# Kernel optimization log

Hardware: AMD Instinct MI355X
Metric: run time of the kernel (lower is better)

Reference implementation:

```python
import jax, jax.numpy as jnp
import numpy as np

NUM_CLASSES = 8   # num_input_classes
BIN_SIZE = 640
K = 16            # num_neighbors
HID = 256         # hidden_dim
DDIM = 128        # distance_dim
MAX_BINS = 200


def setup_inputs() -> dict:
    key = jax.random.key(0)
    ks = jax.random.split(key, 16)
    B, N, F = 4, 12800, 16
    X = jax.random.normal(ks[0], (B, N, F), jnp.float32)
    ids = jax.random.randint(ks[1], (B, N), 0, NUM_CLASSES).astype(jnp.float32)
    X = X.at[:, :, 0].set(ids)
    d_in = NUM_CLASSES + (F - 1)  # 23 after one-hot encoding

    def w(k, shp):
        return jax.random.normal(k, shp, jnp.float32) * 0.05

    return {
        "X": X,
        # point-embedding FFN (layer_encoding): Dense(128, elu) -> Dense(DDIM)
        "We1": w(ks[2], (d_in, 128)), "be1": jnp.zeros((128,), jnp.float32),
        "We2": w(ks[3], (128, DDIM)), "be2": jnp.zeros((DDIM,), jnp.float32),
        # edge FFN (layer_edge): Dense(128, elu) -> Dense(1)
        "Wd1": w(ks[4], (2 * d_in + 1, 128)), "bd1": jnp.zeros((128,), jnp.float32),
        "Wd2": w(ks[5], (128, 1)), "bd2": jnp.zeros((1,), jnp.float32),
        # LSH codebook random rotations (DDIM, max_num_bins//2)
        "R": w(ks[6], (DDIM, MAX_BINS // 2)),
        # encoder dense
        "Wenc": w(ks[7], (d_in, HID)), "benc": jnp.zeros((HID,), jnp.float32),
        # GHConv weights
        "Wt": w(ks[8], (HID, HID)), "bt": jnp.zeros((HID,), jnp.float32),
        "Wh": w(ks[9], (HID, HID)),
        "theta": w(ks[10], (HID, HID)),
        # decoder dense + output head
        "Wdec": w(ks[11], (HID, HID)), "bdec": jnp.zeros((HID,), jnp.float32),
        "Wout": w(ks[12], (HID, 3)), "bout": jnp.zeros((3,), jnp.float32),
    }


def _ffn(x, W1, b1, W2, b2):
    return jax.nn.elu(x @ W1 + b1) @ W2 + b2


def _build_edges(pe, R):
    # pe: (N, DDIM) point embeddings for one event
    N = pe.shape[0]
    nbins = N // BIN_SIZE
    mul = pe @ R[:, : nbins // 2]                      # (N, nbins//2)
    cmul = jnp.concatenate([mul, -mul], axis=-1)       # (N, nbins)
    # LSH binning: argsort of argmax bin id -> (nbins, BIN_SIZE) node indices
    bins = jnp.argsort(jnp.argmax(cmul, axis=-1)).reshape(nbins, BIN_SIZE)
    parts = pe[bins]                                   # (nbins, bs, DDIM)
    dm = jax.nn.sigmoid(jnp.einsum('bif,bjf->bij', parts, parts))
    vals, idx = jax.lax.top_k(dm, K)                   # (nbins, bs, K)
    src = jnp.broadcast_to(bins[:, :, None], (nbins, BIN_SIZE, K)).reshape(-1)
    dst = bins[jnp.arange(nbins)[:, None, None], idx].reshape(-1)
    return src, dst, vals.reshape(-1)


def _ghconv(x, src, dst, w, Wt, bt, Wh, theta):
    # x: (N, HID); edge list (src, dst, w) of length E; out[src] += w * h[dst]
    N = x.shape[0]
    deg = jax.ops.segment_sum(jnp.abs(w), src, num_segments=N)
    norm = (deg + 1e-6) ** -0.5                        # (N,)
    f_hom = (x @ theta) * norm[:, None]
    agg = jax.ops.segment_sum(w[:, None] * f_hom[dst], src, num_segments=N)
    agg = agg * norm[:, None]
    gate = jax.nn.sigmoid(x @ Wt + bt)
    return jax.nn.selu(gate * agg + (1.0 - gate) * (x @ Wh))


def reference(X, We1, be1, We2, be2, Wd1, bd1, Wd2, bd2, R, Wenc, benc, Wt, bt, Wh, theta, Wdec, bdec, Wout, bout):
    # InputEncoding: one-hot the class id, keep remaining properties
    ids = jax.nn.one_hot(X[..., 0].astype(jnp.int32), NUM_CLASSES, dtype=X.dtype)
    h0 = jnp.concatenate([ids, X[..., 1:]], axis=-1)   # (B, N, 23)
    # SparseHashedNNDistance: embed points, LSH-bin, per-bin kNN, edge net
    pe = _ffn(h0, We1, be1, We2, be2)                  # (B, N, DDIM)
    src, dst, d = jax.vmap(lambda p: _build_edges(p, R))(pe)   # each (B, N*K)
    x1 = jax.vmap(lambda h, s: h[s])(h0, src)
    x2 = jax.vmap(lambda h, s: h[s])(h0, dst)
    ef = jnp.concatenate([x1, x2, d[..., None]], axis=-1)      # (B, E, 47)
    w = jax.nn.sigmoid(_ffn(ef, Wd1, bd1, Wd2, bd2))[..., 0]   # (B, E) edge weights
    # EncoderDecoderGNN: Dense encoder -> GHConv -> Dense decoder -> head
    xe = jax.nn.selu(h0 @ Wenc + benc)                 # (B, N, HID)
    xg = jax.vmap(lambda x, s, t, ww: _ghconv(x, s, t, ww, Wt, bt, Wh, theta))(xe, src, dst, w)
    xd = jax.nn.selu(xg @ Wdec + bdec)
    return xd @ Wout + bout                            # (B, N, 3)
```

## Files before the change

### kernel.cpp

```cpp
#include <hip/hip_runtime.h>
#include <cstdint>
#include <cstddef>
#include <math.h>

#define BB    4
#define NN    12800
#define FF    16
#define DIN   23
#define NCLS  8
#define DDIM  128
#define HID   256
#define NBINS 20
#define BS    640
#define KNB   16
#define EE    (NN*KNB)
#define BN    (BB*NN)

__device__ __forceinline__ float eluf(float x){ return x > 0.f ? x : expm1f(x); }
__device__ __forceinline__ float seluf(float x){
  const float a = 1.6732632423543772f, s = 1.0507009873554805f;
  return x > 0.f ? s*x : s*a*expm1f(x);
}
__device__ __forceinline__ float sigf(float x){ return 1.f/(1.f+expf(-x)); }

__global__ void k_h0(const float* __restrict__ X, float* __restrict__ h0){
  int id = blockIdx.x*256 + threadIdx.x;
  if (id >= BN*DIN) return;
  int p = id / DIN, f = id % DIN;
  const float* xr = X + (size_t)p*FF;
  float v;
  if (f < NCLS){
    int cls = (int)xr[0];
    v = (f == cls) ? 1.f : 0.f;
  } else {
    v = xr[f - NCLS + 1];
  }
  h0[id] = v;
}

__global__ void k_pe(const float* __restrict__ h0,
                     const float* __restrict__ We1, const float* __restrict__ be1,
                     const float* __restrict__ We2, const float* __restrict__ be2,
                     float* __restrict__ pe){
  __shared__ double hid[2][128];
  int t = threadIdx.x;
  int lp = t >> 7, j = t & 127;
  size_t p = (size_t)blockIdx.x*2 + lp;
  const float* hr = h0 + p*DIN;
  double acc = (double)be1[j];
  #pragma unroll
  for (int k=0;k<DIN;++k) acc += (double)hr[k]*(double)We1[k*DDIM + j];
  hid[lp][j] = acc > 0.0 ? acc : expm1(acc);
  __syncthreads();
  double acc2 = (double)be2[j];
  #pragma unroll 8
  for (int k=0;k<DDIM;++k) acc2 += hid[lp][k]*(double)We2[k*DDIM + j];
  pe[p*DDIM + j] = (float)acc2;
}

__global__ void k_binid(const float* __restrict__ pe, const float* __restrict__ R,
                        int* __restrict__ bid){
  int tid = blockIdx.x*256 + threadIdx.x;
  int p = tid >> 2, part = tid & 3;
  const float* pr = pe + (size_t)p*DDIM + part*32;
  double m[10];
  #pragma unroll
  for (int j=0;j<10;++j) m[j] = 0.0;
  #pragma unroll 4
  for (int k=0;k<32;++k){
    double v = (double)pr[k];
    const float* rr = R + (size_t)(part*32 + k)*100;
    #pragma unroll
    for (int j=0;j<10;++j) m[j] += v*(double)rr[j];
  }
  #pragma unroll
  for (int j=0;j<10;++j){
    m[j] += __shfl_xor(m[j], 1);
    m[j] += __shfl_xor(m[j], 2);
  }
  if (part == 0){
    float mf[10];
    #pragma unroll
    for (int j=0;j<10;++j) mf[j] = (float)m[j];
    float bv = -1e30f; int bi = 0;
    #pragma unroll
    for (int j=0;j<20;++j){
      float v = (j<10) ? mf[j] : -mf[j-10];
      if (v > bv){ bv = v; bi = j; }
    }
    bid[p] = bi;
  }
}

__global__ void k_place(const int* __restrict__ binid, int* __restrict__ order){
  int b = blockIdx.x / NBINS, mybin = blockIdx.x % NBINS;
  const int* bid = binid + (size_t)b*NN;
  int t = threadIdx.x;
  __shared__ int wsum[4];
  __shared__ int wtot[4];
  __shared__ int sOff;
  int c = 0;
  for (int i = t; i < NN; i += 256) c += (bid[i] < mybin) ? 1 : 0;
  #pragma unroll
  for (int o=32;o;o>>=1) c += __shfl_xor(c, o);
  if ((t & 63) == 0) wsum[t >> 6] = c;
  __syncthreads();
  if (t == 0) sOff = wsum[0]+wsum[1]+wsum[2]+wsum[3];
  __syncthreads();
  int base = sOff;
  int lane = t & 63, w = t >> 6;
  for (int ch = 0; ch < NN; ch += 256){
    int i = ch + t;
    bool flag = (i < NN) && (bid[i] == mybin);
    unsigned long long bal = __ballot(flag);
    int pre = __popcll(bal & ((1ull << lane) - 1ull));
    if (lane == 0) wtot[w] = __popcll(bal);
    __syncthreads();
    int woff = 0;
    #pragma unroll
    for (int ww=0; ww<4; ++ww) if (ww < w) woff += wtot[ww];
    if (flag) order[(size_t)b*NN + base + woff + pre] = i;
    base += wtot[0]+wtot[1]+wtot[2]+wtot[3];
    __syncthreads();
  }
}

#define TP 68
__global__ void __launch_bounds__(256)
k_topk(const float* __restrict__ pe, const int* __restrict__ order,
       float* __restrict__ valk, int* __restrict__ idxk){
  __shared__ float rowT[64][TP];
  __shared__ float colT[64][TP];
  __shared__ float S[64][69];
  __shared__ unsigned short midx[64][48];
  __shared__ int ordRow[64];
  __shared__ int ordCol[64];
  int blk = blockIdx.x;
  int b   = blk / (NBINS*10);
  int rem = blk % (NBINS*10);
  int bin = rem / 10, rt = rem % 10;
  int r0 = rt*64;
  int t = threadIdx.x;
  const float* peb = pe + (size_t)b*NN*DDIM;
  const int* ob = order + (size_t)b*NN + (size_t)bin*BS;
  if (t < 64) ordRow[t] = ob[r0 + t];

  float tv[16]; int ti[16];
  #pragma unroll
  for (int j=0;j<16;++j){ tv[j] = -1e30f; ti[j] = 1<<20; }
  float wv = -1e30f; int wi = 1<<20; int wpos = 0;

  int tm = t & 15, tn = t >> 4;
  int rsel = t & 63, qsel = t >> 6;

  for (int ct = 0; ct < 10; ++ct){
    __syncthreads();
    if (t < 64) ordCol[t] = ob[ct*64 + t];
    double acc[4][4];
    #pragma unroll
    for (int i=0;i<4;++i){
      #pragma unroll
      for (int j=0;j<4;++j) acc[i][j] = 0.0;
    }
    #pragma unroll
    for (int kh = 0; kh < 2; ++kh){
      __syncthreads();
      for (int l=t; l<4096; l+=256){
        int rr = l >> 6, kk = l & 63;
        rowT[kk][rr] = peb[(size_t)ordRow[rr]*DDIM + kh*64 + kk];
      }
      for (int l=t; l<4096; l+=256){
        int cc = l >> 6, kk = l & 63;
        colT[kk][cc] = peb[(size_t)ordCol[cc]*DDIM + kh*64 + kk];
      }
      __syncthreads();
      #pragma unroll 4
      for (int kk=0; kk<64; ++kk){
        float4 a = *(const float4*)&rowT[kk][4*tm];
        float4 w = *(const float4*)&colT[kk][4*tn];
        double ad[4], wd[4];
        ad[0]=(double)a.x; ad[1]=(double)a.y; ad[2]=(double)a.z; ad[3]=(double)a.w;
        wd[0]=(double)w.x; wd[1]=(double)w.y; wd[2]=(double)w.z; wd[3]=(double)w.w;
        #pragma unroll
        for (int i=0;i<4;++i){
          #pragma unroll
          for (int j=0;j<4;++j) acc[i][j] += ad[i]*wd[j];
        }
      }
    }
    #pragma unroll
    for (int i=0;i<4;++i){
      #pragma unroll
      for (int j=0;j<4;++j)
        S[4*tm+i][4*tn+j] = sigf((float)acc[i][j]);
    }
    __syncthreads();
    #pragma unroll
    for (int j=0;j<16;++j){
      float v = S[rsel][qsel*16 + j];
      int gc = ct*64 + qsel*16 + j;
      bool better = (v > wv) || (v == wv && gc < wi);
      if (better){
        #pragma unroll
        for (int u=0;u<16;++u){ if (u == wpos){ tv[u] = v; ti[u] = gc; } }
        wv = tv[0]; wi = ti[0]; wpos = 0;
        #pragma unroll
        for (int u=1;u<16;++u){
          bool worse = (tv[u] < wv) || (tv[u] == wv && ti[u] > wi);
          if (worse){ wv = tv[u]; wi = ti[u]; wpos = u; }
        }
      }
    }
  }
  __syncthreads();
  if (qsel > 0){
    #pragma unroll
    for (int j=0;j<16;++j){
      S[rsel][(qsel-1)*16 + j] = tv[j];
      midx[rsel][(qsel-1)*16 + j] = (unsigned short)ti[j];
    }
  }
  __syncthreads();
  if (qsel == 0){
    for (int j=0;j<48;++j){
      float v = S[rsel][j]; int gc = (int)midx[rsel][j];
      bool better = (v > wv) || (v == wv && gc < wi);
      if (better){
        #pragma unroll
        for (int u=0;u<16;++u){ if (u == wpos){ tv[u] = v; ti[u] = gc; } }
        wv = tv[0]; wi = ti[0]; wpos = 0;
        #pragma unroll
        for (int u=1;u<16;++u){
          bool worse = (tv[u] < wv) || (tv[u] == wv && ti[u] > wi);
          if (worse){ wv = tv[u]; wi = ti[u]; wpos = u; }
        }
      }
    }
    size_t base = (((size_t)(b*NBINS + bin))*BS + r0 + rsel)*KNB;
    #pragma unroll
    for (int j=0;j<16;++j){ valk[base + j] = tv[j]; idxk[base + j] = ti[j]; }
  }
}

__global__ void k_epart(const float* __restrict__ h0,
                        const float* __restrict__ Wd1, const float* __restrict__ bd1,
                        float* __restrict__ spart, float* __restrict__ dpart){
  int t = threadIdx.x;
  int lp = t >> 7, j = t & 127;
  size_t p = (size_t)blockIdx.x*2 + lp;
  const float* hr = h0 + p*DIN;
  float sa = bd1[j];
  float da = 0.f;
  #pragma unroll
  for (int k=0;k<DIN;++k){
    float x = hr[k];
    sa += x*Wd1[k*128 + j];
    da += x*Wd1[(DIN+k)*128 + j];
  }
  spart[p*128 + j] = sa;
  dpart[p*128 + j] = da;
}

__global__ void k_edges(const float* __restrict__ spart, const float* __restrict__ dpart,
                        const int* __restrict__ order,
                        const float* __restrict__ valk, const int* __restrict__ idxk,
                        const float* __restrict__ Wd1, const float* __restrict__ Wd2,
                        const float* __restrict__ bd2,
                        float* __restrict__ wgt, int* __restrict__ dste){
  int lane = threadIdx.x & 63;
  size_t e = (size_t)blockIdx.x*4 + (threadIdx.x >> 6);
  int b  = (int)(e / EE);
  int eb = (int)(e % EE);
  int bin = eb / (BS*KNB);
  int rem = eb % (BS*KNB);
  int i  = rem / KNB;
  int kk = rem % KNB;
  const int* ob = order + (size_t)b*NN + (size_t)bin*BS;
  int src = ob[i];
  size_t tkb = ((size_t)(b*NBINS + bin)*BS + i)*KNB + kk;
  int ip = idxk[tkb];
  int dst = ob[ip];
  float dv = valk[tkb];
  size_t gs = ((size_t)b*NN + src)*128;
  size_t gd = ((size_t)b*NN + dst)*128;
  float a1 = spart[gs + lane]      + dpart[gd + lane]      + dv*Wd1[46*128 + lane];
  float a2 = spart[gs + 64 + lane] + dpart[gd + 64 + lane] + dv*Wd1[46*128 + 64 + lane];
  float ptl = eluf(a1)*Wd2[lane] + eluf(a2)*Wd2[lane + 64];
  #pragma unroll
  for (int o=32;o;o>>=1) ptl += __shfl_xor(ptl, o);
  if (lane == 0){
    wgt[e]  = sigf(ptl + bd2[0]);
    dste[e] = dst;
  }
}

__global__ void k_deg(const float* __restrict__ wgt, const int* __restrict__ order,
                      float* __restrict__ nrm){
  int id = blockIdx.x*256 + threadIdx.x;
  if (id >= BN) return;
  int b = id / NN;
  int p = id % NN;
  const float* w = wgt + (size_t)b*EE + (size_t)p*KNB;
  float s = 0.f;
  #pragma unroll
  for (int k=0;k<KNB;++k) s += fabsf(w[k]);
  int node = order[id];
  nrm[(size_t)b*NN + node] = 1.f/sqrtf(s + 1e-6f);
}

__global__ void k_enc(const float* __restrict__ h0, const float* __restrict__ Wenc,
                      const float* __restrict__ benc, float* __restrict__ xe){
  __shared__ float hs[8][DIN+1];
  size_t p0 = (size_t)blockIdx.x*8;
  int t = threadIdx.x;
  if (t < 8*DIN){
    int pp = t / DIN, ff = t - pp*DIN;
    hs[pp][ff] = h0[(p0+pp)*DIN + ff];
  }
  float wreg[DIN];
  #pragma unroll
  for (int k=0;k<DIN;++k) wreg[k] = Wenc[k*HID + t];
  float bb = benc[t];
  __syncthreads();
  #pragma unroll
  for (int pp=0;pp<8;++pp){
    float acc = bb;
    #pragma unroll
    for (int k=0;k<DIN;++k) acc += hs[pp][k]*wreg[k];
    xe[(p0+pp)*HID + t] = seluf(acc);
  }
}

template<int MODE>
__global__ void __launch_bounds__(256)
k_gemm128(const float* __restrict__ A, const float* __restrict__ W,
          const float* __restrict__ bias, const float* __restrict__ rs,
          float* __restrict__ C){
  __shared__ float As[16][132];
  __shared__ float Ws[16][132];
  int t = threadIdx.x;
  int m0 = blockIdx.x*128, n0 = blockIdx.y*128;
  int tx = t & 15, ty = t >> 4;
  float acc[8][8];
  #pragma unroll
  for (int i=0;i<8;++i){
    #pragma unroll
    for (int j=0;j<8;++j) acc[i][j] = 0.f;
  }
  for (int kt=0; kt<16; ++kt){
    int k0 = kt*16;
    __syncthreads();
    #pragma unroll
    for (int l=0;l<8;++l){
      int idx = t + l*256;
      int m = idx >> 4, kk = idx & 15;
      As[kk][m] = A[((size_t)(m0+m))*HID + k0 + kk];
    }
    #pragma unroll
    for (int l=0;l<8;++l){
      int idx = t + l*256;
      int kk = idx >> 7, nn = idx & 127;
      Ws[kk][nn] = W[((size_t)(k0+kk))*HID + n0 + nn];
    }
    __syncthreads();
    #pragma unroll
    for (int kk=0;kk<16;++kk){
      float4 a0 = *(const float4*)&As[kk][4*ty];
      float4 a1 = *(const float4*)&As[kk][64 + 4*ty];
      float4 w0 = *(const float4*)&Ws[kk][4*tx];
      float4 w1 = *(const float4*)&Ws[kk][64 + 4*tx];
      float av[8], wv[8];
      av[0]=a0.x; av[1]=a0.y; av[2]=a0.z; av[3]=a0.w;
      av[4]=a1.x; av[5]=a1.y; av[6]=a1.z; av[7]=a1.w;
      wv[0]=w0.x; wv[1]=w0.y; wv[2]=w0.z; wv[3]=w0.w;
      wv[4]=w1.x; wv[5]=w1.y; wv[6]=w1.z; wv[7]=w1.w;
      #pragma unroll
      for (int i=0;i<8;++i){
        #pragma unroll
        for (int j=0;j<8;++j) acc[i][j] += av[i]*wv[j];
      }
    }
  }
  float b0[8];
  if (MODE == 2 || MODE == 3){
    #pragma unroll
    for (int j=0;j<8;++j) b0[j] = bias[n0 + (j<4 ? 4*tx+j : 60+4*tx+j)];
  }
  #pragma unroll
  for (int i=0;i<8;++i){
    int row = m0 + (i<4 ? 4*ty+i : 60+4*ty+i);
    float sc = (MODE == 1) ? rs[row] : 1.f;
    float v[8];
    #pragma unroll
    for (int j=0;j<8;++j){
      float x = acc[i][j];
      if (MODE == 2 || MODE == 3) x += b0[j];
      if (MODE == 1) x *= sc;
      if (MODE == 2) x = sigf(x);
      if (MODE == 3) x = seluf(x);
      v[j] = x;
    }
    float4 r0; r0.x=v[0]; r0.y=v[1]; r0.z=v[2]; r0.w=v[3];
    float4 r1; r1.x=v[4]; r1.y=v[5]; r1.z=v[6]; r1.w=v[7];
    *(float4*)&C[(size_t)row*HID + n0 + 4*tx]      = r0;
    *(float4*)&C[(size_t)row*HID + n0 + 64 + 4*tx] = r1;
  }
}

__global__ void k_combine(const float* __restrict__ fh, const float* __restrict__ xh,
                          const float* __restrict__ gate, const float* __restrict__ wgt,
                          const int* __restrict__ dste, const int* __restrict__ order,
                          const float* __restrict__ nrm, float* __restrict__ xg){
  __shared__ float ew[KNB];
  __shared__ int   ed[KNB];
  int blk = blockIdx.x;
  int b = blk / NN, p = blk % NN;
  int t = threadIdx.x;
  if (t < KNB){
    size_t e = (size_t)b*EE + (size_t)p*KNB + t;
    ew[t] = wgt[e];
    ed[t] = dste[e];
  }
  __syncthreads();
  int src = order[(size_t)b*NN + p];
  float nr = nrm[(size_t)b*NN + src];
  size_t base = (size_t)b*NN*HID;
  float acc = 0.f;
  #pragma unroll
  for (int k=0;k<KNB;++k) acc += ew[k]*fh[base + (size_t)ed[k]*HID + t];
  acc *= nr;
  size_t o = base + (size_t)src*HID + t;
  float g = gate[o];
  xg[o] = seluf(g*acc + (1.f - g)*xh[o]);
}

__global__ void k_head(const float* __restrict__ xd, const float* __restrict__ Wout,
                       const float* __restrict__ bout, float* __restrict__ out){
  int lane = threadIdx.x & 63;
  size_t p = (size_t)blockIdx.x*4 + (threadIdx.x >> 6);
  float4 x = *(const float4*)&xd[p*HID + lane*4];
  float a0 = 0.f, a1 = 0.f, a2 = 0.f;
  const float* wr = Wout + lane*4*3;
  a0 += x.x*wr[0]; a1 += x.x*wr[1]; a2 += x.x*wr[2];
  a0 += x.y*wr[3]; a1 += x.y*wr[4]; a2 += x.y*wr[5];
  a0 += x.z*wr[6]; a1 += x.z*wr[7]; a2 += x.z*wr[8];
  a0 += x.w*wr[9]; a1 += x.w*wr[10]; a2 += x.w*wr[11];
  #pragma unroll
  for (int o=32;o;o>>=1){
    a0 += __shfl_xor(a0, o);
    a1 += __shfl_xor(a1, o);
    a2 += __shfl_xor(a2, o);
  }
  if (lane == 0){
    out[p*3 + 0] = a0 + bout[0];
    out[p*3 + 1] = a1 + bout[1];
    out[p*3 + 2] = a2 + bout[2];
  }
}

extern "C" void kernel_launch(void* const* d_in, const int* in_sizes, int n_in,
                              void* d_out, int out_size, void* d_ws, size_t ws_size,
                              hipStream_t stream){
  (void)in_sizes; (void)n_in; (void)out_size; (void)ws_size;
  const float* X    = (const float*)d_in[0];
  const float* We1  = (const float*)d_in[1];
  const float* be1  = (const float*)d_in[2];
  const float* We2  = (const float*)d_in[3];
  const float* be2  = (const float*)d_in[4];
  const float* Wd1  = (const float*)d_in[5];
  const float* bd1  = (const float*)d_in[6];
  const float* Wd2  = (const float*)d_in[7];
  const float* bd2  = (const float*)d_in[8];
  const float* R    = (const float*)d_in[9];
  const float* Wenc = (const float*)d_in[10];
  const float* benc = (const float*)d_in[11];
  const float* Wt   = (const float*)d_in[12];
  const float* bt   = (const float*)d_in[13];
  const float* Wh   = (const float*)d_in[14];
  const float* theta= (const float*)d_in[15];
  const float* Wdec = (const float*)d_in[16];
  const float* bdec = (const float*)d_in[17];
  const float* Wout = (const float*)d_in[18];
  const float* bout = (const float*)d_in[19];
  float* out = (float*)d_out;

  char* ws = (char*)d_ws; size_t off = 0;
  auto alloc = [&](size_t bytes)->void*{
    void* p = ws + off; off = (off + bytes + 255) & ~(size_t)255; return p;
  };
  float* h0   = (float*)alloc((size_t)BN*DIN*4);
  float* pe   = (float*)alloc((size_t)BN*DDIM*4);
  int*   bid  = (int*)  alloc((size_t)BN*4);
  int*   order= (int*)  alloc((size_t)BN*4);
  float* valk = (float*)alloc((size_t)BB*NBINS*BS*KNB*4);
  int*   idxk = (int*)  alloc((size_t)BB*NBINS*BS*KNB*4);
  float* wgt  = (float*)alloc((size_t)BB*EE*4);
  int*   dste = (int*)  alloc((size_t)BB*EE*4);
  float* nrm  = (float*)alloc((size_t)BN*4);
  float* xe   = (float*)alloc((size_t)BN*HID*4);
  float* fh   = (float*)alloc((size_t)BN*HID*4);
  float* xh   = (float*)alloc((size_t)BN*HID*4);
  float* gate = (float*)alloc((size_t)BN*HID*4);
  float* spart = pe;
  float* dpart = xe;
  float* xg    = xe;
  float* xd    = fh;

  k_h0   <<<(BN*DIN + 255)/256, 256, 0, stream>>>(X, h0);
  k_pe   <<<BN/2, 256, 0, stream>>>(h0, We1, be1, We2, be2, pe);
  k_binid<<<BN*4/256, 256, 0, stream>>>(pe, R, bid);
  k_place<<<BB*NBINS, 256, 0, stream>>>(bid, order);
  k_topk <<<BB*NBINS*10, 256, 0, stream>>>(pe, order, valk, idxk);
  k_epart<<<BN/2, 256, 0, stream>>>(h0, Wd1, bd1, spart, dpart);
  k_edges<<<BB*EE/4, 256, 0, stream>>>(spart, dpart, order, valk, idxk, Wd1, Wd2, bd2, wgt, dste);
  k_deg  <<<(BN + 255)/256, 256, 0, stream>>>(wgt, order, nrm);
  k_enc  <<<BN/8, 256, 0, stream>>>(h0, Wenc, benc, xe);
  dim3 gg(BN/128, HID/128);
  k_gemm128<0><<<gg, 256, 0, stream>>>(xe, Wh,    nullptr, nullptr, xh);
  k_gemm128<1><<<gg, 256, 0, stream>>>(xe, theta, nullptr, nrm,     fh);
  k_gemm128<2><<<gg, 256, 0, stream>>>(xe, Wt,    bt,      nullptr, gate);
  k_combine<<<BN, 256, 0, stream>>>(fh, xh, gate, wgt, dste, order, nrm, xg);
  k_gemm128<3><<<gg, 256, 0, stream>>>(xg, Wdec,  bdec,    nullptr, xd);
  k_head <<<BN/4, 256, 0, stream>>>(xd, Wout, bout, out);
}
```

Measured before the change: 1.814 ms.

## Remap topk tile so each thread owns one row's 16 columns

Changes the thread-to-output mapping in the per-bin kNN kernel: each thread now computes 16 consecutive column scores for a single row instead of a 4x4 tile. The scores feed the thread's running top-16 directly from registers, which removes the shared score matrix S, its write/read pass and one barrier per column tile. The merge buffers reuse the rowT/colT shared memory, cutting the LDS footprint and possibly raising occupancy. In exchange, data reuse per LDS load drops (1 row value per 16 FMAs instead of 4x4 outer products), so more LDS traffic goes to the fp64 FMAs.

```diff
diff --git a/kernel.cpp b/kernel.cpp
--- a/kernel.cpp
+++ b/kernel.cpp
@@ -125,14 +125,12 @@
   }
 }
 
-#define TP 68
+#define TPAD 68
 __global__ void __launch_bounds__(256)
 k_topk(const float* __restrict__ pe, const int* __restrict__ order,
        float* __restrict__ valk, int* __restrict__ idxk){
-  __shared__ float rowT[64][TP];
-  __shared__ float colT[64][TP];
-  __shared__ float S[64][69];
-  __shared__ unsigned short midx[64][48];
+  __shared__ float rowT[64][TPAD];
+  __shared__ float colT[64][TPAD];
   __shared__ int ordRow[64];
   __shared__ int ordCol[64];
   int blk = blockIdx.x;
@@ -141,6 +139,8 @@
   int bin = rem / 10, rt = rem % 10;
   int r0 = rt*64;
   int t = threadIdx.x;
+  int lane = t & 63;
+  int q    = t >> 6;
   const float* peb = pe + (size_t)b*NN*DDIM;
   const int* ob = order + (size_t)b*NN + (size_t)bin*BS;
   if (t < 64) ordRow[t] = ob[r0 + t];
@@ -150,18 +150,11 @@
   for (int j=0;j<16;++j){ tv[j] = -1e30f; ti[j] = 1<<20; }
   float wv = -1e30f; int wi = 1<<20; int wpos = 0;
 
-  int tm = t & 15, tn = t >> 4;
-  int rsel = t & 63, qsel = t >> 6;
-
   for (int ct = 0; ct < 10; ++ct){
-    __syncthreads();
     if (t < 64) ordCol[t] = ob[ct*64 + t];
-    double acc[4][4];
-    #pragma unroll
-    for (int i=0;i<4;++i){
-      #pragma unroll
-      for (int j=0;j<4;++j) acc[i][j] = 0.0;
-    }
+    double acc[16];
+    #pragma unroll
+    for (int j=0;j<16;++j) acc[j] = 0.0;
     #pragma unroll
     for (int kh = 0; kh < 2; ++kh){
       __syncthreads();
@@ -174,31 +167,27 @@
         colT[kk][cc] = peb[(size_t)ordCol[cc]*DDIM + kh*64 + kk];
       }
       __syncthreads();
-      #pragma unroll 4
+      #pragma unroll 2
       for (int kk=0; kk<64; ++kk){
-        float4 a = *(const float4*)&rowT[kk][4*tm];
-        float4 w = *(const float4*)&colT[kk][4*tn];
-        double ad[4], wd[4];
-        ad[0]=(double)a.x; ad[1]=(double)a.y; ad[2]=(double)a.z; ad[3]=(double)a.w;
-        wd[0]=(double)w.x; wd[1]=(double)w.y; wd[2]=(double)w.z; wd[3]=(double)w.w;
-        #pragma unroll
-        for (int i=0;i<4;++i){
-          #pragma unroll
-          for (int j=0;j<4;++j) acc[i][j] += ad[i]*wd[j];
-        }
+        double a = (double)rowT[kk][lane];
+        float4 w0 = *(const float4*)&colT[kk][16*q];
+        float4 w1 = *(const float4*)&colT[kk][16*q + 4];
+        float4 w2 = *(const float4*)&colT[kk][16*q + 8];
+        float4 w3 = *(const float4*)&colT[kk][16*q + 12];
+        acc[0]  += a*(double)w0.x; acc[1]  += a*(double)w0.y;
+        acc[2]  += a*(double)w0.z; acc[3]  += a*(double)w0.w;
+        acc[4]  += a*(double)w1.x; acc[5]  += a*(double)w1.y;
+        acc[6]  += a*(double)w1.z; acc[7]  += a*(double)w1.w;
+        acc[8]  += a*(double)w2.x; acc[9]  += a*(double)w2.y;
+        acc[10] += a*(double)w2.z; acc[11] += a*(double)w2.w;
+        acc[12] += a*(double)w3.x; acc[13] += a*(double)w3.y;
+        acc[14] += a*(double)w3.z; acc[15] += a*(double)w3.w;
       }
     }
     #pragma unroll
-    for (int i=0;i<4;++i){
-      #pragma unroll
-      for (int j=0;j<4;++j)
-        S[4*tm+i][4*tn+j] = sigf((float)acc[i][j]);
-    }
-    __syncthreads();
-    #pragma unroll
     for (int j=0;j<16;++j){
-      float v = S[rsel][qsel*16 + j];
-      int gc = ct*64 + qsel*16 + j;
+      float v = sigf((float)acc[j]);
+      int gc = ct*64 + 16*q + j;
       bool better = (v > wv) || (v == wv && gc < wi);
       if (better){
         #pragma unroll
@@ -213,17 +202,21 @@
     }
   }
   __syncthreads();
-  if (qsel > 0){
+  float* mv = (float*)&rowT[0][0];
+  int*   mi = (int*)  &colT[0][0];
+  const int MS = 49;
+  if (q > 0){
     #pragma unroll
     for (int j=0;j<16;++j){
-      S[rsel][(qsel-1)*16 + j] = tv[j];
-      midx[rsel][(qsel-1)*16 + j] = (unsigned short)ti[j];
-    }
-  }
-  __syncthreads();
-  if (qsel == 0){
+      mv[lane*MS + (q-1)*16 + j] = tv[j];
+      mi[lane*MS + (q-1)*16 + j] = ti[j];
+    }
+  }
+  __syncthreads();
+  if (q == 0){
     for (int j=0;j<48;++j){
-      float v = S[rsel][j]; int gc = (int)midx[rsel][j];
+      float v = mv[lane*MS + j];
+      int gc  = mi[lane*MS + j];
       bool better = (v > wv) || (v == wv && gc < wi);
       if (better){
         #pragma unroll
@@ -236,7 +229,7 @@
         }
       }
     }
-    size_t base = (((size_t)(b*NBINS + bin))*BS + r0 + rsel)*KNB;
+    size_t base = (((size_t)(b*NBINS + bin))*BS + r0 + lane)*KNB;
     #pragma unroll
     for (int j=0;j<16;++j){ valk[base + j] = tv[j]; idxk[base + j] = ti[j]; }
   }
```

Measured after the change: 1.746 ms. -3.8%, faster.

## Use fp32 accumulation in topk GEMM, load row tile once, reuse shared memory

Applied to the files above, without the earlier changes.

Switches the per-bin similarity accumulation in k_topk from double to float, which is much cheaper on the FP32 ALUs. The full 128-dim row tile is now staged into shared memory once per block instead of being reloaded on every column tile. The score matrix and merge buffers are aliased onto existing shared arrays to keep LDS usage down. The risk is that fp32 rounding can reorder near-tied neighbours relative to the double-precision version.

```diff
diff --git a/kernel.cpp b/kernel.cpp
--- a/kernel.cpp
+++ b/kernel.cpp
@@ -125,14 +125,12 @@
   }
 }
 
-#define TP 68
+#define TPAD 68
 __global__ void __launch_bounds__(256)
 k_topk(const float* __restrict__ pe, const int* __restrict__ order,
        float* __restrict__ valk, int* __restrict__ idxk){
-  __shared__ float rowT[64][TP];
-  __shared__ float colT[64][TP];
-  __shared__ float S[64][69];
-  __shared__ unsigned short midx[64][48];
+  __shared__ float rowF[128][TPAD];
+  __shared__ float colT[64][TPAD];
   __shared__ int ordRow[64];
   __shared__ int ordCol[64];
   int blk = blockIdx.x;
@@ -141,34 +139,35 @@
   int bin = rem / 10, rt = rem % 10;
   int r0 = rt*64;
   int t = threadIdx.x;
+  int tm = t & 15, tn = t >> 4;
+  int rsel = t & 63, qsel = t >> 6;
   const float* peb = pe + (size_t)b*NN*DDIM;
   const int* ob = order + (size_t)b*NN + (size_t)bin*BS;
   if (t < 64) ordRow[t] = ob[r0 + t];
+  __syncthreads();
+  for (int l=t; l<8192; l+=256){
+    int rr = l >> 7, kk = l & 127;
+    rowF[kk][rr] = peb[(size_t)ordRow[rr]*DDIM + kk];
+  }
 
   float tv[16]; int ti[16];
   #pragma unroll
   for (int j=0;j<16;++j){ tv[j] = -1e30f; ti[j] = 1<<20; }
   float wv = -1e30f; int wi = 1<<20; int wpos = 0;
 
-  int tm = t & 15, tn = t >> 4;
-  int rsel = t & 63, qsel = t >> 6;
+  float (*S_T)[TPAD] = colT;
 
   for (int ct = 0; ct < 10; ++ct){
-    __syncthreads();
     if (t < 64) ordCol[t] = ob[ct*64 + t];
-    double acc[4][4];
+    float acc[4][4];
     #pragma unroll
     for (int i=0;i<4;++i){
       #pragma unroll
-      for (int j=0;j<4;++j) acc[i][j] = 0.0;
+      for (int j=0;j<4;++j) acc[i][j] = 0.f;
     }
     #pragma unroll
     for (int kh = 0; kh < 2; ++kh){
       __syncthreads();
-      for (int l=t; l<4096; l+=256){
-        int rr = l >> 6, kk = l & 63;
-        rowT[kk][rr] = peb[(size_t)ordRow[rr]*DDIM + kh*64 + kk];
-      }
       for (int l=t; l<4096; l+=256){
         int cc = l >> 6, kk = l & 63;
         colT[kk][cc] = peb[(size_t)ordCol[cc]*DDIM + kh*64 + kk];
@@ -176,28 +175,25 @@
       __syncthreads();
       #pragma unroll 4
       for (int kk=0; kk<64; ++kk){
-        float4 a = *(const float4*)&rowT[kk][4*tm];
+        float4 a = *(const float4*)&rowF[kh*64 + kk][4*tm];
         float4 w = *(const float4*)&colT[kk][4*tn];
-        double ad[4], wd[4];
-        ad[0]=(double)a.x; ad[1]=(double)a.y; ad[2]=(double)a.z; ad[3]=(double)a.w;
-        wd[0]=(double)w.x; wd[1]=(double)w.y; wd[2]=(double)w.z; wd[3]=(double)w.w;
-        #pragma unroll
-        for (int i=0;i<4;++i){
-          #pragma unroll
-          for (int j=0;j<4;++j) acc[i][j] += ad[i]*wd[j];
-        }
+        acc[0][0]+=a.x*w.x; acc[0][1]+=a.x*w.y; acc[0][2]+=a.x*w.z; acc[0][3]+=a.x*w.w;
+        acc[1][0]+=a.y*w.x; acc[1][1]+=a.y*w.y; acc[1][2]+=a.y*w.z; acc[1][3]+=a.y*w.w;
+        acc[2][0]+=a.z*w.x; acc[2][1]+=a.z*w.y; acc[2][2]+=a.z*w.z; acc[2][3]+=a.z*w.w;
+        acc[3][0]+=a.w*w.x; acc[3][1]+=a.w*w.y; acc[3][2]+=a.w*w.z; acc[3][3]+=a.w*w.w;
       }
     }
+    __syncthreads();
     #pragma unroll
     for (int i=0;i<4;++i){
       #pragma unroll
       for (int j=0;j<4;++j)
-        S[4*tm+i][4*tn+j] = sigf((float)acc[i][j]);
+        S_T[4*tn+j][4*tm+i] = sigf(acc[i][j]);
     }
     __syncthreads();
     #pragma unroll
     for (int j=0;j<16;++j){
-      float v = S[rsel][qsel*16 + j];
+      float v = S_T[qsel*16 + j][rsel];
       int gc = ct*64 + qsel*16 + j;
       bool better = (v > wv) || (v == wv && gc < wi);
       if (better){
@@ -213,17 +209,21 @@
     }
   }
   __syncthreads();
+  float* mv = (float*)&rowF[0][0];
+  int*   mi = (int*)  &rowF[64][0];
+  const int MS = 49;
   if (qsel > 0){
     #pragma unroll
     for (int j=0;j<16;++j){
-      S[rsel][(qsel-1)*16 + j] = tv[j];
-      midx[rsel][(qsel-1)*16 + j] = (unsigned short)ti[j];
+      mv[rsel*MS + (qsel-1)*16 + j] = tv[j];
+      mi[rsel*MS + (qsel-1)*16 + j] = ti[j];
     }
   }
   __syncthreads();
   if (qsel == 0){
     for (int j=0;j<48;++j){
-      float v = S[rsel][j]; int gc = (int)midx[rsel][j];
+      float v = mv[rsel*MS + j];
+      int gc  = mi[rsel*MS + j];
       bool better = (v > wv) || (v == wv && gc < wi);
       if (better){
         #pragma unroll
```

New measurement: 1.619 ms. 10.7% less time.
